# Optimization experiments

Hardware: AMD Instinct MI355X
Metric: run time of the kernel (lower is better)

Reference implementation:

```python
import jax, jax.numpy as jnp
import numpy as np

N_NODES = 50000
N_EDGES = 150000
NODE_F, EDGE_F = 4, 11
HID, HID_OUT = 512, 1024
VS, AS_, N_ACT = 2048, 2048, 1000


def _graph_conv(x, W, b, src, dst, n, edge_weight=None):
    # DGL GraphConv, norm='both': D_out^{-1/2} on src feats, sum-aggregate, D_in^{-1/2} on dst.
    deg_out = jnp.maximum(jnp.zeros((n,), x.dtype).at[src].add(1.0), 1.0)
    deg_in = jnp.maximum(jnp.zeros((n,), x.dtype).at[dst].add(1.0), 1.0)
    h = x * (deg_out[:, None] ** -0.5)
    mult_first = W.shape[0] > W.shape[1]
    if mult_first:
        h = h @ W
    m = h[src]  # [E, d] gather
    if edge_weight is not None:
        m = m * edge_weight  # elementwise u_mul_e
    agg = jax.ops.segment_sum(m, dst, num_segments=n)
    if not mult_first:
        agg = agg @ W
    return agg * (deg_in[:, None] ** -0.5) + b


def setup_inputs() -> dict:
    key = jax.random.key(0)
    ks = jax.random.split(key, 16)
    s = 0.05
    return {
        'node_feats': jax.random.normal(ks[0], (N_NODES, NODE_F), jnp.float32),
        'edge_feats': jax.random.normal(ks[1], (N_EDGES, EDGE_F), jnp.float32),
        'W1': jax.random.normal(ks[2], (NODE_F, EDGE_F), jnp.float32) * s,
        'b1': jnp.zeros((EDGE_F,), jnp.float32),
        'W2': jax.random.normal(ks[3], (EDGE_F, HID), jnp.float32) * s,
        'b2': jnp.zeros((HID,), jnp.float32),
        'W3': jax.random.normal(ks[4], (HID, HID_OUT), jnp.float32) * s,
        'b3': jnp.zeros((HID_OUT,), jnp.float32),
        'Wv1': jax.random.normal(ks[5], (HID_OUT, VS), jnp.float32) * s,
        'bv1': jnp.zeros((VS,), jnp.float32),
        'Wv2': jax.random.normal(ks[6], (VS, 1), jnp.float32) * s,
        'bv2': jnp.zeros((1,), jnp.float32),
        'Wa1': jax.random.normal(ks[7], (HID_OUT, AS_), jnp.float32) * s,
        'ba1': jnp.zeros((AS_,), jnp.float32),
        'Wa2': jax.random.normal(ks[8], (AS_, N_ACT), jnp.float32) * s,
        'ba2': jnp.zeros((N_ACT,), jnp.float32),
        'src': jax.random.randint(ks[9], (N_EDGES,), 0, N_NODES, jnp.int32),
        'dst': jax.random.randint(ks[10], (N_EDGES,), 0, N_NODES, jnp.int32),
    }


def reference(node_feats, edge_feats, W1, b1, W2, b2, W3, b3,
              Wv1, bv1, Wv2, bv2, Wa1, ba1, Wa2, ba2, src, dst):
    n = node_feats.shape[0]
    loop = jnp.arange(n, dtype=src.dtype)
    srcL = jnp.concatenate([src, loop])  # add_self_loop
    dstL = jnp.concatenate([dst, loop])
    # self-loop edges get zero edge features (DGL default)
    ef = jnp.concatenate([edge_feats, jnp.zeros((n, edge_feats.shape[1]), edge_feats.dtype)], axis=0)

    h = jax.nn.relu(_graph_conv(node_feats, W1, b1, srcL, dstL, n))          # [N, 11]
    h = jax.nn.relu(_graph_conv(h, W2, b2, srcL, dstL, n, edge_weight=ef))   # [N, 512]
    h = _graph_conv(h, W3, b3, srcL, dstL, n)                                # [N, 1024]

    g_emb = jnp.mean(h, axis=0, keepdims=True)  # dgl.mean_nodes, single graph -> [1, 1024]

    v = jax.nn.relu(g_emb @ Wv1 + bv1) @ Wv2 + bv2        # [1, 1]
    a = jax.nn.relu(g_emb @ Wa1 + ba1) @ Wa2 + ba2        # [1, N_ACT]
    return v + (a - a.mean())
```

## Files before the change

### kernel.cpp

```cpp
#include <hip/hip_runtime.h>

#define NN 50000
#define NE 150000
#define NB 196

__global__ __launch_bounds__(256) void k_deg(const int* __restrict__ src,
                                             const int* __restrict__ dst,
                                             int* __restrict__ deg_out,
                                             int* __restrict__ deg_in) {
    int e = blockIdx.x * 256 + threadIdx.x;
    if (e < NE) {
        atomicAdd(&deg_out[src[e]], 1);
        atomicAdd(&deg_in[dst[e]], 1);
    }
}

__global__ __launch_bounds__(256) void k_bsum(const int* __restrict__ deg_in,
                                              const int* __restrict__ deg_out,
                                              int* __restrict__ bsum_in,
                                              int* __restrict__ bsum_out) {
    __shared__ int si[256], so[256];
    int t = threadIdx.x;
    int idx = blockIdx.x * 256 + t;
    si[t] = (idx < NN) ? deg_in[idx] : 0;
    so[t] = (idx < NN) ? deg_out[idx] : 0;
    __syncthreads();
    for (int off = 128; off >= 1; off >>= 1) {
        if (t < off) { si[t] += si[t + off]; so[t] += so[t + off]; }
        __syncthreads();
    }
    if (t == 0) { bsum_in[blockIdx.x] = si[0]; bsum_out[blockIdx.x] = so[0]; }
}

__global__ __launch_bounds__(256) void k_rowptr(const int* __restrict__ deg_in,
                                                const int* __restrict__ deg_out,
                                                const int* __restrict__ bsum_in,
                                                const int* __restrict__ bsum_out,
                                                int* __restrict__ rp_in,
                                                int* __restrict__ rp_out) {
    __shared__ int si[256], so[256];
    int b = blockIdx.x, t = threadIdx.x;
    si[t] = (t < b) ? bsum_in[t] : 0;
    so[t] = (t < b) ? bsum_out[t] : 0;
    __syncthreads();
    for (int off = 128; off >= 1; off >>= 1) {
        if (t < off) { si[t] += si[t + off]; so[t] += so[t + off]; }
        __syncthreads();
    }
    int off_in = si[0], off_out = so[0];
    __syncthreads();
    int idx = b * 256 + t;
    int di = (idx < NN) ? deg_in[idx] : 0;
    int dq = (idx < NN) ? deg_out[idx] : 0;
    si[t] = di; so[t] = dq;
    __syncthreads();
    for (int off = 1; off < 256; off <<= 1) {
        int a = (t >= off) ? si[t - off] : 0;
        int c2 = (t >= off) ? so[t - off] : 0;
        __syncthreads();
        si[t] += a; so[t] += c2;
        __syncthreads();
    }
    if (idx < NN) {
        rp_in[idx]  = off_in  + si[t] - di;
        rp_out[idx] = off_out + so[t] - dq;
    }
    if (b == 0 && t == 0) { rp_in[NN] = NE; rp_out[NN] = NE; }
}

__global__ __launch_bounds__(256) void k_scatter(const int* __restrict__ src,
                                                 const int* __restrict__ dst,
                                                 const int* __restrict__ rp_in,
                                                 const int* __restrict__ rp_out,
                                                 int* __restrict__ cur_in,
                                                 int* __restrict__ cur_out,
                                                 int* __restrict__ eidx_in,
                                                 int* __restrict__ nbr_out) {
    int e = blockIdx.x * 256 + threadIdx.x;
    if (e >= NE) return;
    int s = src[e], d = dst[e];
    int pi = rp_in[d] + atomicAdd(&cur_in[d], 1);
    eidx_in[pi] = e;
    int po = rp_out[s] + atomicAdd(&cur_out[s], 1);
    nbr_out[po] = d;
}

__global__ __launch_bounds__(256) void k_conv1g(const float* __restrict__ x,
                                                const int* __restrict__ src,
                                                const int* __restrict__ eidx_in,
                                                const int* __restrict__ rp_in,
                                                const int* __restrict__ nbr_out,
                                                const int* __restrict__ rp_out,
                                                const int* __restrict__ deg_out,
                                                const int* __restrict__ deg_in,
                                                const float* __restrict__ W1,
                                                const float* __restrict__ b1,
                                                float* __restrict__ h1s,
                                                float* __restrict__ c) {
    int n = blockIdx.x * 256 + threadIdx.x;
    if (n >= NN) return;
    float din  = rsqrtf((float)(deg_in[n] + 1));
    float dout = rsqrtf((float)(deg_out[n] + 1));
    const float4 xn = ((const float4*)x)[n];
    float a0 = xn.x * dout, a1 = xn.y * dout, a2 = xn.z * dout, a3 = xn.w * dout;
    int beg = rp_in[n], end = rp_in[n + 1];
    for (int p = beg; p < end; p++) {
        int e = eidx_in[p];
        int s = src[e];
        float ds = rsqrtf((float)(deg_out[s] + 1));
        float4 xs = ((const float4*)x)[s];
        a0 = fmaf(xs.x, ds, a0);
        a1 = fmaf(xs.y, ds, a1);
        a2 = fmaf(xs.z, ds, a2);
        a3 = fmaf(xs.w, ds, a3);
    }
    float cacc = din;
    int ob = rp_out[n], oe = rp_out[n + 1];
    for (int p = ob; p < oe; p++) {
        int d = nbr_out[p];
        cacc += rsqrtf((float)(deg_in[d] + 1));
    }
    c[n] = cacc;
    #pragma unroll
    for (int j = 0; j < 11; j++) {
        float y = a0 * W1[0 * 11 + j] + a1 * W1[1 * 11 + j] +
                  a2 * W1[2 * 11 + j] + a3 * W1[3 * 11 + j];
        y = fmaxf(fmaf(y, din, b1[j]), 0.f);
        h1s[n * 11 + j] = y * dout;
    }
}

__global__ __launch_bounds__(256) void k_agg2g(const float* __restrict__ h1s,
                                               const float* __restrict__ ef,
                                               const int* __restrict__ src,
                                               const int* __restrict__ eidx_in,
                                               const int* __restrict__ rp_in,
                                               float* __restrict__ agg2) {
    int tid = threadIdx.x;
    if (tid >= 253) return;
    int n = blockIdx.x * 23 + tid / 11;
    int j = tid % 11;
    if (n >= NN) return;
    int beg = rp_in[n], end = rp_in[n + 1];
    float acc = 0.f;
    for (int p = beg; p < end; p++) {
        int e = eidx_in[p];
        int s = src[e];
        acc = fmaf(h1s[s * 11 + j], ef[e * 11 + j], acc);
    }
    agg2[n * 11 + j] = acc;
}

#define NPB 64
__global__ __launch_bounds__(512) void k_conv2_reduce(const float* __restrict__ agg2,
                                                      const float* __restrict__ W2,
                                                      const float* __restrict__ b2,
                                                      const float* __restrict__ c,
                                                      const int* __restrict__ deg_out,
                                                      const int* __restrict__ deg_in,
                                                      float* __restrict__ t) {
    __shared__ float tile[NPB * 11];
    __shared__ float din_sh[NPB], w_sh[NPB];
    int n0 = blockIdx.x * NPB;
    int tid = threadIdx.x;
    for (int i = tid; i < NPB * 11; i += 512) {
        int gi = n0 * 11 + i;
        tile[i] = (gi < NN * 11) ? agg2[gi] : 0.f;
    }
    if (tid < NPB) {
        int node = n0 + tid;
        if (node < NN) {
            din_sh[tid] = rsqrtf((float)(deg_in[node] + 1));
            w_sh[tid]   = c[node] * rsqrtf((float)(deg_out[node] + 1)) * (1.0f / NN);
        } else { din_sh[tid] = 0.f; w_sh[tid] = 0.f; }
    }
    __syncthreads();
    float w[11];
    #pragma unroll
    for (int j = 0; j < 11; j++) w[j] = W2[j * 512 + tid];
    float bias = b2[tid];
    float acc = 0.f;
    for (int i = 0; i < NPB; i++) {
        float dot = 0.f;
        #pragma unroll
        for (int j = 0; j < 11; j++) dot = fmaf(tile[i * 11 + j], w[j], dot);
        float y = fmaxf(fmaf(dot, din_sh[i], bias), 0.f);
        acc = fmaf(w_sh[i], y, acc);
    }
    atomicAdd(&t[tid], acc);
}

__global__ __launch_bounds__(256) void k_g(const float* __restrict__ t,
                                           const float* __restrict__ W3,
                                           const float* __restrict__ b3,
                                           float* __restrict__ g) {
    int b = blockIdx.x;
    int oc = b & 3, kc = b >> 2;
    int o = oc * 256 + threadIdx.x;
    int k0 = kc * 32;
    __shared__ float ts[32];
    if (threadIdx.x < 32) ts[threadIdx.x] = t[k0 + threadIdx.x];
    __syncthreads();
    float acc = (kc == 0) ? b3[o] : 0.f;
    #pragma unroll 8
    for (int k = 0; k < 32; k++) acc = fmaf(ts[k], W3[(size_t)(k0 + k) * 1024 + o], acc);
    atomicAdd(&g[o], acc);
}

__global__ __launch_bounds__(256) void k_heads1(const float* __restrict__ g,
                                                const float* __restrict__ Wv1,
                                                const float* __restrict__ Wa1,
                                                float* __restrict__ hv_raw,
                                                float* __restrict__ ha_raw) {
    int b = blockIdx.x;
    int oc = b >> 4, kc = b & 15;
    int idx = oc * 256 + threadIdx.x;
    int k0 = kc * 64;
    __shared__ float gs[64];
    if (threadIdx.x < 64) gs[threadIdx.x] = g[k0 + threadIdx.x];
    __syncthreads();
    const float* W; float* outp; int o;
    if (idx < 2048) { W = Wv1; outp = hv_raw; o = idx; }
    else            { W = Wa1; outp = ha_raw; o = idx - 2048; }
    float acc = 0.f;
    #pragma unroll 8
    for (int k = 0; k < 64; k++) acc = fmaf(gs[k], W[(size_t)(k0 + k) * 2048 + o], acc);
    atomicAdd(&outp[o], acc);
}

__global__ __launch_bounds__(256) void k_heads2(const float* __restrict__ hv_raw,
                                                const float* __restrict__ bv1,
                                                const float* __restrict__ ha_raw,
                                                const float* __restrict__ ba1,
                                                const float* __restrict__ Wv2,
                                                const float* __restrict__ bv2,
                                                const float* __restrict__ Wa2,
                                                float* __restrict__ a_acc,
                                                float* __restrict__ v) {
    int b = blockIdx.x;
    int tid = threadIdx.x;
    if (b < 128) {
        int oc = b >> 5, kc = b & 31;
        int k0 = kc * 64;
        __shared__ float hs[64];
        if (tid < 64) hs[tid] = fmaxf(ha_raw[k0 + tid] + ba1[k0 + tid], 0.f);
        __syncthreads();
        int o = oc * 256 + tid;
        if (o < 1000) {
            float acc = 0.f;
            #pragma unroll 8
            for (int k = 0; k < 64; k++)
                acc = fmaf(hs[k], Wa2[(size_t)(k0 + k) * 1000 + o], acc);
            atomicAdd(&a_acc[o], acc);
        }
    } else {
        __shared__ float red[256];
        float acc = 0.f;
        for (int k = tid; k < 2048; k += 256)
            acc = fmaf(fmaxf(hv_raw[k] + bv1[k], 0.f), Wv2[k], acc);
        red[tid] = acc;
        __syncthreads();
        for (int s = 128; s >= 1; s >>= 1) {
            if (tid < s) red[tid] += red[tid + s];
            __syncthreads();
        }
        if (tid == 0) *v = red[0] + bv2[0];
    }
}

__global__ __launch_bounds__(1024) void k_final(const float* __restrict__ a_acc,
                                                const float* __restrict__ ba2,
                                                const float* __restrict__ vptr,
                                                float* __restrict__ out) {
    __shared__ float red[1024];
    int tid = threadIdx.x;
    float ai = (tid < 1000) ? a_acc[tid] + ba2[tid] : 0.f;
    red[tid] = ai;
    __syncthreads();
    for (int s = 512; s >= 1; s >>= 1) {
        if (tid < s) red[tid] += red[tid + s];
        __syncthreads();
    }
    float amean = red[0] * (1.0f / 1000.0f);
    if (tid < 1000) out[tid] = vptr[0] + ai - amean;
}

extern "C" void kernel_launch(void* const* d_in, const int* in_sizes, int n_in,
                              void* d_out, int out_size, void* d_ws, size_t ws_size,
                              hipStream_t stream) {
    const float* x   = (const float*)d_in[0];
    const float* ef  = (const float*)d_in[1];
    const float* W1  = (const float*)d_in[2];
    const float* b1  = (const float*)d_in[3];
    const float* W2  = (const float*)d_in[4];
    const float* b2  = (const float*)d_in[5];
    const float* W3  = (const float*)d_in[6];
    const float* b3  = (const float*)d_in[7];
    const float* Wv1 = (const float*)d_in[8];
    const float* bv1 = (const float*)d_in[9];
    const float* Wv2 = (const float*)d_in[10];
    const float* bv2 = (const float*)d_in[11];
    const float* Wa1 = (const float*)d_in[12];
    const float* ba1 = (const float*)d_in[13];
    const float* Wa2 = (const float*)d_in[14];
    const float* ba2 = (const float*)d_in[15];
    const int*   src = (const int*)d_in[16];
    const int*   dst = (const int*)d_in[17];
    float* out = (float*)d_out;

    char* ws = (char*)d_ws;
    size_t off = 0;
    auto alloc = [&](size_t bytes) -> void* {
        void* p = ws + off;
        off = (off + bytes + 255) & ~(size_t)255;
        return p;
    };
    int*   deg_out = (int*)  alloc(NN * 4);
    int*   deg_in  = (int*)  alloc(NN * 4);
    int*   cur_in  = (int*)  alloc(NN * 4);
    int*   cur_out = (int*)  alloc(NN * 4);
    float* t       = (float*)alloc(512 * 4);
    float* g       = (float*)alloc(1024 * 4);
    float* hv_raw  = (float*)alloc(2048 * 4);
    float* ha_raw  = (float*)alloc(2048 * 4);
    float* a_acc   = (float*)alloc(1024 * 4);
    size_t zero_bytes = off;
    int*   bsum_in  = (int*)  alloc(NB * 4);
    int*   bsum_out = (int*)  alloc(NB * 4);
    int*   rp_in    = (int*)  alloc((NN + 1) * 4);
    int*   rp_out   = (int*)  alloc((NN + 1) * 4);
    int*   eidx_in  = (int*)  alloc((size_t)NE * 4);
    int*   nbr_out  = (int*)  alloc((size_t)NE * 4);
    float* c        = (float*)alloc(NN * 4);
    float* h1s      = (float*)alloc((size_t)NN * 11 * 4);
    float* agg2     = (float*)alloc((size_t)NN * 11 * 4);
    float* v        = (float*)alloc(256);

    hipMemsetAsync(d_ws, 0, zero_bytes, stream);

    k_deg<<<(NE + 255) / 256, 256, 0, stream>>>(src, dst, deg_out, deg_in);
    k_bsum<<<NB, 256, 0, stream>>>(deg_in, deg_out, bsum_in, bsum_out);
    k_rowptr<<<NB, 256, 0, stream>>>(deg_in, deg_out, bsum_in, bsum_out, rp_in, rp_out);
    k_scatter<<<(NE + 255) / 256, 256, 0, stream>>>(src, dst, rp_in, rp_out,
                                                    cur_in, cur_out, eidx_in, nbr_out);
    k_conv1g<<<(NN + 255) / 256, 256, 0, stream>>>(x, src, eidx_in, rp_in, nbr_out, rp_out,
                                                   deg_out, deg_in, W1, b1, h1s, c);
    k_agg2g<<<(NN + 22) / 23, 256, 0, stream>>>(h1s, ef, src, eidx_in, rp_in, agg2);
    k_conv2_reduce<<<(NN + NPB - 1) / NPB, 512, 0, stream>>>(agg2, W2, b2, c, deg_out, deg_in, t);
    k_g<<<64, 256, 0, stream>>>(t, W3, b3, g);
    k_heads1<<<256, 256, 0, stream>>>(g, Wv1, Wa1, hv_raw, ha_raw);
    k_heads2<<<129, 256, 0, stream>>>(hv_raw, bv1, ha_raw, ba1, Wv2, bv2, Wa2, a_acc, v);
    k_final<<<1, 1024, 0, stream>>>(a_acc, ba2, v, out);
}
```

Baseline: 205.6 us.

## Precompute degree norms, pack edge/src indices, fuse conv2 aggregation and reduction

Computes rsqrt-normalised in/out degrees and pre-scaled node features once in the rowptr kernel, so the later per-edge loops no longer recompute rsqrt. The CSR now stores an (edge, src) pair per slot, which removes the dependent src[e] load. The edge-weighted aggregation for conv2 is fused into the reduction kernel, dropping the agg2 buffer and one launch, with fewer nodes per block. The split-K head GEMVs get more blocks with smaller K chunks, which adds more atomics in exchange for more parallelism.

```diff
diff --git a/kernel.cpp b/kernel.cpp
--- a/kernel.cpp
+++ b/kernel.cpp
@@ -36,8 +36,12 @@
                                                 const int* __restrict__ deg_out,
                                                 const int* __restrict__ bsum_in,
                                                 const int* __restrict__ bsum_out,
+                                                const float* __restrict__ x,
                                                 int* __restrict__ rp_in,
-                                                int* __restrict__ rp_out) {
+                                                int* __restrict__ rp_out,
+                                                float* __restrict__ dins,
+                                                float* __restrict__ douts,
+                                                float4* __restrict__ xs4) {
     __shared__ int si[256], so[256];
     int b = blockIdx.x, t = threadIdx.x;
     si[t] = (t < b) ? bsum_in[t] : 0;
@@ -64,6 +68,13 @@
     if (idx < NN) {
         rp_in[idx]  = off_in  + si[t] - di;
         rp_out[idx] = off_out + so[t] - dq;
+        float dif = rsqrtf((float)(di + 1));
+        float dqf = rsqrtf((float)(dq + 1));
+        dins[idx] = dif;
+        douts[idx] = dqf;
+        float4 x4 = ((const float4*)x)[idx];
+        x4.x *= dqf; x4.y *= dqf; x4.z *= dqf; x4.w *= dqf;
+        xs4[idx] = x4;
     }
     if (b == 0 && t == 0) { rp_in[NN] = NE; rp_out[NN] = NE; }
 }
@@ -74,105 +85,87 @@
                                                  const int* __restrict__ rp_out,
                                                  int* __restrict__ cur_in,
                                                  int* __restrict__ cur_out,
-                                                 int* __restrict__ eidx_in,
+                                                 int2* __restrict__ ei_pack,
                                                  int* __restrict__ nbr_out) {
     int e = blockIdx.x * 256 + threadIdx.x;
     if (e >= NE) return;
     int s = src[e], d = dst[e];
     int pi = rp_in[d] + atomicAdd(&cur_in[d], 1);
-    eidx_in[pi] = e;
+    ei_pack[pi] = make_int2(e, s);
     int po = rp_out[s] + atomicAdd(&cur_out[s], 1);
     nbr_out[po] = d;
 }
 
-__global__ __launch_bounds__(256) void k_conv1g(const float* __restrict__ x,
-                                                const int* __restrict__ src,
-                                                const int* __restrict__ eidx_in,
+__global__ __launch_bounds__(256) void k_conv1g(const float4* __restrict__ xs4,
+                                                const int2* __restrict__ ei_pack,
                                                 const int* __restrict__ rp_in,
                                                 const int* __restrict__ nbr_out,
                                                 const int* __restrict__ rp_out,
-                                                const int* __restrict__ deg_out,
-                                                const int* __restrict__ deg_in,
+                                                const float* __restrict__ dins,
+                                                const float* __restrict__ douts,
                                                 const float* __restrict__ W1,
                                                 const float* __restrict__ b1,
                                                 float* __restrict__ h1s,
                                                 float* __restrict__ c) {
     int n = blockIdx.x * 256 + threadIdx.x;
     if (n >= NN) return;
-    float din  = rsqrtf((float)(deg_in[n] + 1));
-    float dout = rsqrtf((float)(deg_out[n] + 1));
-    const float4 xn = ((const float4*)x)[n];
-    float a0 = xn.x * dout, a1 = xn.y * dout, a2 = xn.z * dout, a3 = xn.w * dout;
+    float din  = dins[n];
+    float dout = douts[n];
+    float4 a = xs4[n];
     int beg = rp_in[n], end = rp_in[n + 1];
     for (int p = beg; p < end; p++) {
-        int e = eidx_in[p];
-        int s = src[e];
-        float ds = rsqrtf((float)(deg_out[s] + 1));
-        float4 xs = ((const float4*)x)[s];
-        a0 = fmaf(xs.x, ds, a0);
-        a1 = fmaf(xs.y, ds, a1);
-        a2 = fmaf(xs.z, ds, a2);
-        a3 = fmaf(xs.w, ds, a3);
+        int s = ei_pack[p].y;
+        float4 xs = xs4[s];
+        a.x += xs.x; a.y += xs.y; a.z += xs.z; a.w += xs.w;
     }
     float cacc = din;
     int ob = rp_out[n], oe = rp_out[n + 1];
-    for (int p = ob; p < oe; p++) {
-        int d = nbr_out[p];
-        cacc += rsqrtf((float)(deg_in[d] + 1));
-    }
+    for (int p = ob; p < oe; p++)
+        cacc += dins[nbr_out[p]];
     c[n] = cacc;
     #pragma unroll
     for (int j = 0; j < 11; j++) {
-        float y = a0 * W1[0 * 11 + j] + a1 * W1[1 * 11 + j] +
-                  a2 * W1[2 * 11 + j] + a3 * W1[3 * 11 + j];
+        float y = a.x * W1[0 * 11 + j] + a.y * W1[1 * 11 + j] +
+                  a.z * W1[2 * 11 + j] + a.w * W1[3 * 11 + j];
         y = fmaxf(fmaf(y, din, b1[j]), 0.f);
         h1s[n * 11 + j] = y * dout;
     }
 }
 
-__global__ __launch_bounds__(256) void k_agg2g(const float* __restrict__ h1s,
-                                               const float* __restrict__ ef,
-                                               const int* __restrict__ src,
-                                               const int* __restrict__ eidx_in,
-                                               const int* __restrict__ rp_in,
-                                               float* __restrict__ agg2) {
+#define G2 32
+__global__ __launch_bounds__(512) void k_conv2f(const float* __restrict__ h1s,
+                                                const float* __restrict__ ef,
+                                                const int2* __restrict__ ei_pack,
+                                                const int* __restrict__ rp_in,
+                                                const float* __restrict__ c,
+                                                const float* __restrict__ dins,
+                                                const float* __restrict__ douts,
+                                                const float* __restrict__ W2,
+                                                const float* __restrict__ b2,
+                                                float* __restrict__ t) {
+    __shared__ float tile[G2 * 11];
+    __shared__ float din_sh[G2], w_sh[G2];
+    int n0 = blockIdx.x * G2;
     int tid = threadIdx.x;
-    if (tid >= 253) return;
-    int n = blockIdx.x * 23 + tid / 11;
-    int j = tid % 11;
-    if (n >= NN) return;
-    int beg = rp_in[n], end = rp_in[n + 1];
-    float acc = 0.f;
-    for (int p = beg; p < end; p++) {
-        int e = eidx_in[p];
-        int s = src[e];
-        acc = fmaf(h1s[s * 11 + j], ef[e * 11 + j], acc);
-    }
-    agg2[n * 11 + j] = acc;
-}
-
-#define NPB 64
-__global__ __launch_bounds__(512) void k_conv2_reduce(const float* __restrict__ agg2,
-                                                      const float* __restrict__ W2,
-                                                      const float* __restrict__ b2,
-                                                      const float* __restrict__ c,
-                                                      const int* __restrict__ deg_out,
-                                                      const int* __restrict__ deg_in,
-                                                      float* __restrict__ t) {
-    __shared__ float tile[NPB * 11];
-    __shared__ float din_sh[NPB], w_sh[NPB];
-    int n0 = blockIdx.x * NPB;
-    int tid = threadIdx.x;
-    for (int i = tid; i < NPB * 11; i += 512) {
-        int gi = n0 * 11 + i;
-        tile[i] = (gi < NN * 11) ? agg2[gi] : 0.f;
-    }
-    if (tid < NPB) {
-        int node = n0 + tid;
-        if (node < NN) {
-            din_sh[tid] = rsqrtf((float)(deg_in[node] + 1));
-            w_sh[tid]   = c[node] * rsqrtf((float)(deg_out[node] + 1)) * (1.0f / NN);
-        } else { din_sh[tid] = 0.f; w_sh[tid] = 0.f; }
+    if (tid < G2 * 11) {
+        int i = tid / 11, j = tid % 11;
+        int n = n0 + i;
+        float acc = 0.f;
+        if (n < NN) {
+            int beg = rp_in[n], end = rp_in[n + 1];
+            for (int p = beg; p < end; p++) {
+                int2 es = ei_pack[p];
+                acc = fmaf(h1s[es.y * 11 + j], ef[es.x * 11 + j], acc);
+            }
+        }
+        tile[tid] = acc;
+    } else if (tid >= 512 - G2) {
+        int i = tid - (512 - G2);
+        int n = n0 + i;
+        if (n < NN) {
+            din_sh[i] = dins[n];
+            w_sh[i]   = c[n] * douts[n] * (1.0f / NN);
+        } else { din_sh[i] = 0.f; w_sh[i] = 0.f; }
     }
     __syncthreads();
     float w[11];
@@ -180,7 +173,7 @@
     for (int j = 0; j < 11; j++) w[j] = W2[j * 512 + tid];
     float bias = b2[tid];
     float acc = 0.f;
-    for (int i = 0; i < NPB; i++) {
+    for (int i = 0; i < G2; i++) {
         float dot = 0.f;
         #pragma unroll
         for (int j = 0; j < 11; j++) dot = fmaf(tile[i * 11 + j], w[j], dot);
@@ -197,13 +190,13 @@
     int b = blockIdx.x;
     int oc = b & 3, kc = b >> 2;
     int o = oc * 256 + threadIdx.x;
-    int k0 = kc * 32;
-    __shared__ float ts[32];
-    if (threadIdx.x < 32) ts[threadIdx.x] = t[k0 + threadIdx.x];
+    int k0 = kc * 16;
+    __shared__ float ts[16];
+    if (threadIdx.x < 16) ts[threadIdx.x] = t[k0 + threadIdx.x];
     __syncthreads();
     float acc = (kc == 0) ? b3[o] : 0.f;
-    #pragma unroll 8
-    for (int k = 0; k < 32; k++) acc = fmaf(ts[k], W3[(size_t)(k0 + k) * 1024 + o], acc);
+    #pragma unroll
+    for (int k = 0; k < 16; k++) acc = fmaf(ts[k], W3[(size_t)(k0 + k) * 1024 + o], acc);
     atomicAdd(&g[o], acc);
 }
 
@@ -213,18 +206,18 @@
                                                 float* __restrict__ hv_raw,
                                                 float* __restrict__ ha_raw) {
     int b = blockIdx.x;
-    int oc = b >> 4, kc = b & 15;
+    int oc = b >> 5, kc = b & 31;
     int idx = oc * 256 + threadIdx.x;
-    int k0 = kc * 64;
-    __shared__ float gs[64];
-    if (threadIdx.x < 64) gs[threadIdx.x] = g[k0 + threadIdx.x];
+    int k0 = kc * 32;
+    __shared__ float gs[32];
+    if (threadIdx.x < 32) gs[threadIdx.x] = g[k0 + threadIdx.x];
     __syncthreads();
     const float* W; float* outp; int o;
     if (idx < 2048) { W = Wv1; outp = hv_raw; o = idx; }
     else            { W = Wa1; outp = ha_raw; o = idx - 2048; }
     float acc = 0.f;
     #pragma unroll 8
-    for (int k = 0; k < 64; k++) acc = fmaf(gs[k], W[(size_t)(k0 + k) * 2048 + o], acc);
+    for (int k = 0; k < 32; k++) acc = fmaf(gs[k], W[(size_t)(k0 + k) * 2048 + o], acc);
     atomicAdd(&outp[o], acc);
 }
 
@@ -239,17 +232,17 @@
                                                 float* __restrict__ v) {
     int b = blockIdx.x;
     int tid = threadIdx.x;
-    if (b < 128) {
-        int oc = b >> 5, kc = b & 31;
-        int k0 = kc * 64;
-        __shared__ float hs[64];
-        if (tid < 64) hs[tid] = fmaxf(ha_raw[k0 + tid] + ba1[k0 + tid], 0.f);
+    if (b < 256) {
+        int oc = b >> 6, kc = b & 63;
+        int k0 = kc * 32;
+        __shared__ float hs[32];
+        if (tid < 32) hs[tid] = fmaxf(ha_raw[k0 + tid] + ba1[k0 + tid], 0.f);
         __syncthreads();
         int o = oc * 256 + tid;
         if (o < 1000) {
             float acc = 0.f;
             #pragma unroll 8
-            for (int k = 0; k < 64; k++)
+            for (int k = 0; k < 32; k++)
                 acc = fmaf(hs[k], Wa2[(size_t)(k0 + k) * 1000 + o], acc);
             atomicAdd(&a_acc[o], acc);
         }
@@ -325,30 +318,33 @@
     float* ha_raw  = (float*)alloc(2048 * 4);
     float* a_acc   = (float*)alloc(1024 * 4);
     size_t zero_bytes = off;
-    int*   bsum_in  = (int*)  alloc(NB * 4);
-    int*   bsum_out = (int*)  alloc(NB * 4);
-    int*   rp_in    = (int*)  alloc((NN + 1) * 4);
-    int*   rp_out   = (int*)  alloc((NN + 1) * 4);
-    int*   eidx_in  = (int*)  alloc((size_t)NE * 4);
-    int*   nbr_out  = (int*)  alloc((size_t)NE * 4);
-    float* c        = (float*)alloc(NN * 4);
-    float* h1s      = (float*)alloc((size_t)NN * 11 * 4);
-    float* agg2     = (float*)alloc((size_t)NN * 11 * 4);
-    float* v        = (float*)alloc(256);
+    int*    bsum_in  = (int*)   alloc(NB * 4);
+    int*    bsum_out = (int*)   alloc(NB * 4);
+    int*    rp_in    = (int*)   alloc((NN + 1) * 4);
+    int*    rp_out   = (int*)   alloc((NN + 1) * 4);
+    float*  dins     = (float*) alloc(NN * 4);
+    float*  douts    = (float*) alloc(NN * 4);
+    float4* xs4      = (float4*)alloc((size_t)NN * 16);
+    int2*   ei_pack  = (int2*)  alloc((size_t)NE * 8);
+    int*    nbr_out  = (int*)   alloc((size_t)NE * 4);
+    float*  c        = (float*) alloc(NN * 4);
+    float*  h1s      = (float*) alloc((size_t)NN * 11 * 4);
+    float*  v        = (float*) alloc(256);
 
     hipMemsetAsync(d_ws, 0, zero_bytes, stream);
 
     k_deg<<<(NE + 255) / 256, 256, 0, stream>>>(src, dst, deg_out, deg_in);
     k_bsum<<<NB, 256, 0, stream>>>(deg_in, deg_out, bsum_in, bsum_out);
-    k_rowptr<<<NB, 256, 0, stream>>>(deg_in, deg_out, bsum_in, bsum_out, rp_in, rp_out);
+    k_rowptr<<<NB, 256, 0, stream>>>(deg_in, deg_out, bsum_in, bsum_out, x,
+                                     rp_in, rp_out, dins, douts, xs4);
     k_scatter<<<(NE + 255) / 256, 256, 0, stream>>>(src, dst, rp_in, rp_out,
-                                                    cur_in, cur_out, eidx_in, nbr_out);
-    k_conv1g<<<(NN + 255) / 256, 256, 0, stream>>>(x, src, eidx_in, rp_in, nbr_out, rp_out,
-                                                   deg_out, deg_in, W1, b1, h1s, c);
-    k_agg2g<<<(NN + 22) / 23, 256, 0, stream>>>(h1s, ef, src, eidx_in, rp_in, agg2);
-    k_conv2_reduce<<<(NN + NPB - 1) / NPB, 512, 0, stream>>>(agg2, W2, b2, c, deg_out, deg_in, t);
-    k_g<<<64, 256, 0, stream>>>(t, W3, b3, g);
-    k_heads1<<<256, 256, 0, stream>>>(g, Wv1, Wa1, hv_raw, ha_raw);
-    k_heads2<<<129, 256, 0, stream>>>(hv_raw, bv1, ha_raw, ba1, Wv2, bv2, Wa2, a_acc, v);
+                                                    cur_in, cur_out, ei_pack, nbr_out);
+    k_conv1g<<<(NN + 255) / 256, 256, 0, stream>>>(xs4, ei_pack, rp_in, nbr_out, rp_out,
+                                                   dins, douts, W1, b1, h1s, c);
+    k_conv2f<<<(NN + G2 - 1) / G2, 512, 0, stream>>>(h1s, ef, ei_pack, rp_in, c,
+                                                     dins, douts, W2, b2, t);
+    k_g<<<128, 256, 0, stream>>>(t, W3, b3, g);
+    k_heads1<<<512, 256, 0, stream>>>(g, Wv1, Wa1, hv_raw, ha_raw);
+    k_heads2<<<257, 256, 0, stream>>>(hv_raw, bv1, ha_raw, ba1, Wv2, bv2, Wa2, a_acc, v);
     k_final<<<1, 1024, 0, stream>>>(a_acc, ba2, v, out);
 }
```

After: 214.5 us. 1.04x slower.
